# Optimization experiments

Hardware: AMD Instinct MI355X
Metric: run time of the kernel (lower is better)

The kernel has to match this reference:

```python
import jax, jax.numpy as jnp
import numpy as np

B, H, W, DIM, NH = 2, 48, 48, 768, 12
HD = DIM // NH  # 64


def setup_inputs() -> dict:
    key = jax.random.key(0)
    ks = jax.random.split(key, 7)
    std = 0.02
    return {
        "x": jax.random.normal(ks[0], (B, H, W, DIM), jnp.float32),
        "rel_pos_h": jax.random.normal(ks[1], (2 * H - 1, HD), jnp.float32) * std,
        "rel_pos_w": jax.random.normal(ks[2], (2 * W - 1, HD), jnp.float32) * std,
        "qkv_w": jax.random.normal(ks[3], (3 * DIM, DIM), jnp.float32) * std,
        "qkv_b": jnp.zeros((3 * DIM,), jnp.float32),
        "proj_w": jax.random.normal(ks[4], (DIM, DIM), jnp.float32) * std,
        "proj_b": jnp.zeros((DIM,), jnp.float32),
    }


def reference(x, rel_pos_h, rel_pos_w, qkv_w, qkv_b, proj_w, proj_b):
    b, h, w, dim = x.shape
    nh = NH
    hd = dim // nh
    scale = hd ** -0.5
    n = h * w
    # qkv projection: (B,N,3*dim) -> (3, B*nh, N, hd)
    qkv = x.reshape(b, n, dim) @ qkv_w.T + qkv_b
    qkv = qkv.reshape(b, n, 3, nh, hd).transpose(2, 0, 3, 1, 4).reshape(3, b * nh, n, hd)
    q, k, v = qkv[0], qkv[1], qkv[2]
    # scaled dot-product scores (B*nh, N, N)
    attn = jnp.einsum('bnc,bmc->bnm', q * scale, k)
    # decomposed relative position bias (q_size == k_size, no interpolation)
    idx_h = jnp.arange(h)[:, None] - jnp.arange(h)[None, :] + (h - 1)  # (h,h)
    idx_w = jnp.arange(w)[:, None] - jnp.arange(w)[None, :] + (w - 1)  # (w,w)
    Rh = rel_pos_h[idx_h]  # (h, h, hd)
    Rw = rel_pos_w[idx_w]  # (w, w, hd)
    r_q = q.reshape(b * nh, h, w, hd)
    rel_h = jnp.einsum('bhwc,hkc->bhwk', r_q, Rh)  # (B*nh, h, w, h)
    rel_w = jnp.einsum('bhwc,wkc->bhwk', r_q, Rw)  # (B*nh, h, w, w)
    attn = (attn.reshape(b * nh, h, w, h, w)
            + rel_h[:, :, :, :, None]
            + rel_w[:, :, :, None, :]).reshape(b * nh, n, n)
    attn = jax.nn.softmax(attn, axis=-1)
    out = (attn @ v).reshape(b, nh, h, w, hd).transpose(0, 2, 3, 1, 4).reshape(b, h, w, dim)
    return out @ proj_w.T + proj_b
```

## Files before the change

kernel.cpp:

```cpp
#include <hip/hip_runtime.h>
#include <hip/hip_bf16.h>
#include <stdint.h>

#define NQ    2304
#define MROWS 4608
#define DIMC  768
#define NHEAD 12
#define HEADS 24
#define HD    64

typedef unsigned int uint;
typedef unsigned short u16;
typedef __attribute__((ext_vector_type(8))) short s16x8;
typedef __attribute__((ext_vector_type(4))) float f32x4;

#define MFMA16(a, b, c) __builtin_amdgcn_mfma_f32_16x16x32_bf16((a), (b), (c), 0, 0, 0)

static __device__ __forceinline__ float bfbits2f(uint u) {
  union { uint i; float f; } c; c.i = u << 16; return c.f;
}
static __device__ __forceinline__ u16 f2bf(float f) {
  __hip_bfloat16 h = __float2bfloat16(f);
  union { __hip_bfloat16 h; u16 u; } c; c.h = h; return c.u;
}
static __device__ __forceinline__ u16 f2h(float f) {
  union { _Float16 h; u16 u; } c; c.h = (_Float16)f; return c.u;
}
static __device__ __forceinline__ float h2f(u16 u) {
  union { u16 u; _Float16 h; } c; c.u = u; return (float)c.h;
}
static __device__ __forceinline__ void dec8(uint4 p, float* f) {
  f[0] = bfbits2f(p.x & 0xFFFFu); f[1] = bfbits2f(p.x >> 16);
  f[2] = bfbits2f(p.y & 0xFFFFu); f[3] = bfbits2f(p.y >> 16);
  f[4] = bfbits2f(p.z & 0xFFFFu); f[5] = bfbits2f(p.z >> 16);
  f[6] = bfbits2f(p.w & 0xFFFFu); f[7] = bfbits2f(p.w >> 16);
}
static __device__ __forceinline__ void ld8(const void* p, size_t idx, int bf, float* f) {
  if (bf) { dec8(*(const uint4*)((const u16*)p + idx), f); }
  else {
    const float4* q = (const float4*)((const float*)p + idx);
    float4 a = q[0], b = q[1];
    f[0] = a.x; f[1] = a.y; f[2] = a.z; f[3] = a.w;
    f[4] = b.x; f[5] = b.y; f[6] = b.z; f[7] = b.w;
  }
}
static __device__ __forceinline__ float ld1(const void* p, size_t idx, int bf) {
  return bf ? bfbits2f(((const u16*)p)[idx]) : ((const float*)p)[idx];
}
static __device__ __forceinline__ uint4 ld8_to_bf(const void* p, size_t idx, int bf) {
  if (bf) return *(const uint4*)((const u16*)p + idx);
  float f[8]; ld8(p, idx, 0, f);
  uint4 u;
  u.x = (uint)f2bf(f[0]) | ((uint)f2bf(f[1]) << 16);
  u.y = (uint)f2bf(f[2]) | ((uint)f2bf(f[3]) << 16);
  u.z = (uint)f2bf(f[4]) | ((uint)f2bf(f[5]) << 16);
  u.w = (uint)f2bf(f[6]) | ((uint)f2bf(f[7]) << 16);
  return u;
}

__global__ __launch_bounds__(256) void detect_k(const u16* __restrict__ x,
                                                int* __restrict__ mode) {
  __shared__ int wsum[4];
  int t = threadIdx.x;
  int cnt = 0;
  for (int i = 0; i < 8; ++i) {
    uint u = x[(size_t)(t * 8 + i) * 2];
    uint e = (u >> 7) & 0xFFu;
    uint mag = u & 0x7FFFu;
    if (mag == 0 || (e >= 113 && e <= 133)) cnt++;
  }
#pragma unroll
  for (int d = 1; d < 64; d <<= 1) cnt += __shfl_xor(cnt, d);
  if ((t & 63) == 0) wsum[t >> 6] = cnt;
  __syncthreads();
  if (t == 0) mode[0] = ((wsum[0] + wsum[1] + wsum[2] + wsum[3]) > 1024) ? 1 : 0;
}

#define NX8 442368u
#define NW8 221184u
#define NP8 73728u
__global__ __launch_bounds__(256) void convert_k(
    const void* __restrict__ x, const void* __restrict__ qkvw,
    const void* __restrict__ pw, const int* __restrict__ mode,
    u16* __restrict__ xb, u16* __restrict__ wb, u16* __restrict__ pwb)
{
  const int bf = mode[0];
  uint i8 = blockIdx.x * 256 + threadIdx.x;
  if (i8 < NX8) {
    *(uint4*)(xb + (size_t)i8 * 8) = ld8_to_bf(x, (size_t)i8 * 8, bf);
  } else if (i8 < NX8 + NW8) {
    size_t j = i8 - NX8;
    *(uint4*)(wb + j * 8) = ld8_to_bf(qkvw, j * 8, bf);
  } else if (i8 < NX8 + NW8 + NP8) {
    size_t j = i8 - NX8 - NW8;
    *(uint4*)(pwb + j * 8) = ld8_to_bf(pw, j * 8, bf);
  }
}

__global__ __launch_bounds__(256) void qkv_gemm_k(
    const u16* __restrict__ Xb, const u16* __restrict__ Wb,
    const void* __restrict__ Bq, const int* __restrict__ mode,
    u16* __restrict__ Q, u16* __restrict__ K, u16* __restrict__ V)
{
  __shared__ __align__(16) u16 As[128][40];
  __shared__ __align__(16) u16 Bs[128][40];
  const int bf = mode[0];
  const int t = threadIdx.x;
  const int w = t >> 6, l15 = t & 15, quad = (t >> 4) & 3;
  const int wr = w >> 1, wc = w & 1;
  const int row0 = blockIdx.y << 7, col0 = blockIdx.x << 7;
  const int lr = t >> 1, lk = (t & 1) << 4;

  f32x4 zero4 = {0.f, 0.f, 0.f, 0.f};
  f32x4 acc[4][4];
#pragma unroll
  for (int i = 0; i < 4; ++i)
#pragma unroll
    for (int j = 0; j < 4; ++j) acc[i][j] = zero4;

  for (int kt = 0; kt < DIMC; kt += 32) {
    __syncthreads();
    *(uint4*)&As[lr][lk]     = *(const uint4*)(Xb + (size_t)(row0 + lr) * DIMC + kt + lk);
    *(uint4*)&As[lr][lk + 8] = *(const uint4*)(Xb + (size_t)(row0 + lr) * DIMC + kt + lk + 8);
    *(uint4*)&Bs[lr][lk]     = *(const uint4*)(Wb + (size_t)(col0 + lr) * DIMC + kt + lk);
    *(uint4*)&Bs[lr][lk + 8] = *(const uint4*)(Wb + (size_t)(col0 + lr) * DIMC + kt + lk + 8);
    __syncthreads();
    s16x8 af[4], bfr[4];
#pragma unroll
    for (int i = 0; i < 4; ++i)
      af[i] = *(const s16x8*)&As[(wr << 6) + (i << 4) + l15][quad << 3];
#pragma unroll
    for (int j = 0; j < 4; ++j)
      bfr[j] = *(const s16x8*)&Bs[(wc << 6) + (j << 4) + l15][quad << 3];
#pragma unroll
    for (int i = 0; i < 4; ++i)
#pragma unroll
      for (int j = 0; j < 4; ++j)
        acc[i][j] = MFMA16(af[i], bfr[j], acc[i][j]);
  }

#pragma unroll
  for (int jt = 0; jt < 4; ++jt) {
    int col = col0 + (wc << 6) + (jt << 4) + l15;
    int which = col / DIMC;
    int rem = col - which * DIMC;
    int head = rem >> 6, d = rem & 63;
    float bv = ld1(Bq, col, bf);
    u16* dst = (which == 0) ? Q : (which == 1) ? K : V;
#pragma unroll
    for (int i = 0; i < 4; ++i)
#pragma unroll
      for (int r = 0; r < 4; ++r) {
        int mrow = row0 + (wr << 6) + (i << 4) + (quad << 2) + r;
        int b_ = (mrow >= NQ) ? 1 : 0;
        int n = mrow - b_ * NQ;
        dst[(((size_t)(b_ * NHEAD + head)) * NQ + n) * HD + d] = f2bf(acc[i][jt][r] + bv);
      }
  }
}

__global__ __launch_bounds__(256) void vtrans_k(
    const u16* __restrict__ V, u16* __restrict__ Vt)
{
  __shared__ __align__(16) u16 L[64][72];
  const int blk = blockIdx.x;
  const int bhd = blk / 36;
  const int n0 = (blk - bhd * 36) << 6;
  const int t = threadIdx.x;
  const int r = t >> 3, c8 = (t & 7) << 3;

  const u16* src = V + ((size_t)bhd * NQ + n0) * HD;
  *(uint4*)&L[r][c8]      = *(const uint4*)(src + (size_t)r * HD + c8);
  *(uint4*)&L[r + 32][c8] = *(const uint4*)(src + (size_t)(r + 32) * HD + c8);
  __syncthreads();

  u16* dst = Vt + (size_t)bhd * HD * NQ + n0;
#pragma unroll
  for (int half = 0; half < 2; ++half) {
    int d = r + (half << 5);
    u16 tmp[8];
#pragma unroll
    for (int j = 0; j < 8; ++j) tmp[j] = L[c8 + j][d];
    *(uint4*)(dst + (size_t)d * NQ + c8) = *(uint4*)tmp;
  }
}

__global__ __launch_bounds__(256) void bias_gemm_k(
    const u16* __restrict__ Qw,
    const void* __restrict__ rph, const void* __restrict__ rpw,
    const int* __restrict__ mode,
    u16* __restrict__ Bh_g, u16* __restrict__ Bw_g)
{
  __shared__ __align__(16) u16 As[128][72];
  __shared__ __align__(16) u16 Bs[192][72];
  const int bf = mode[0];
  const int t = threadIdx.x;
  const int w = t >> 6, l15 = t & 15, quad = (t >> 4) & 3;
  const int wr = w >> 1, wc = w & 1;
  const int blk = blockIdx.x;
  const int bhd = blk / 18;
  const int row0 = (blk - bhd * 18) << 7;

  {
    int lr = t >> 1, lk = (t & 1) << 5;
    const u16* src = Qw + ((size_t)bhd * NQ + row0 + lr) * HD + lk;
    *(uint4*)&As[lr][lk]      = *(const uint4*)(src);
    *(uint4*)&As[lr][lk + 8]  = *(const uint4*)(src + 8);
    *(uint4*)&As[lr][lk + 16] = *(const uint4*)(src + 16);
    *(uint4*)&As[lr][lk + 24] = *(const uint4*)(src + 24);
  }
  for (int e = t; e < 384; e += 256) {
    int row = e >> 1, k32 = (e & 1) << 5;
    int tab = (row >= 96) ? 1 : 0;
    int r2 = row - (tab ? 96 : 0);
    if (r2 > 94) r2 = 0;
    const void* src = tab ? rpw : rph;
    *(uint4*)&Bs[row][k32]      = ld8_to_bf(src, (size_t)r2 * HD + k32, bf);
    *(uint4*)&Bs[row][k32 + 8]  = ld8_to_bf(src, (size_t)r2 * HD + k32 + 8, bf);
    *(uint4*)&Bs[row][k32 + 16] = ld8_to_bf(src, (size_t)r2 * HD + k32 + 16, bf);
    *(uint4*)&Bs[row][k32 + 24] = ld8_to_bf(src, (size_t)r2 * HD + k32 + 24, bf);
  }
  __syncthreads();

  f32x4 zero4 = {0.f, 0.f, 0.f, 0.f};
  f32x4 acc[4][6];
#pragma unroll
  for (int i = 0; i < 4; ++i)
#pragma unroll
    for (int j = 0; j < 6; ++j) acc[i][j] = zero4;

#pragma unroll
  for (int ks = 0; ks < 2; ++ks) {
    s16x8 af[4], bfr[6];
#pragma unroll
    for (int i = 0; i < 4; ++i)
      af[i] = *(const s16x8*)&As[(wr << 6) + (i << 4) + l15][(ks << 5) + (quad << 3)];
#pragma unroll
    for (int j = 0; j < 6; ++j)
      bfr[j] = *(const s16x8*)&Bs[wc * 96 + (j << 4) + l15][(ks << 5) + (quad << 3)];
#pragma unroll
    for (int i = 0; i < 4; ++i)
#pragma unroll
      for (int j = 0; j < 6; ++j)
        acc[i][j] = MFMA16(af[i], bfr[j], acc[i][j]);
  }

#pragma unroll
  for (int jt = 0; jt < 6; ++jt) {
    int col = wc * 96 + (jt << 4) + l15;
    int tab = (col >= 96) ? 1 : 0;
    int j = col - (tab ? 96 : 0);
    if (j >= 95) continue;
    u16* dstT = tab ? Bw_g : Bh_g;
#pragma unroll
    for (int i = 0; i < 4; ++i)
#pragma unroll
      for (int r = 0; r < 4; ++r) {
        int n = row0 + (wr << 6) + (i << 4) + (quad << 2) + r;
        int qh = (n * 10923) >> 19;
        int coord = tab ? (n - qh * 48) : qh;
        int c = coord + 47 - j;
        if (c >= 0 && c < 48)
          dstT[((size_t)bhd * 48 + c) * NQ + n] = f2h(acc[i][jt][r]);
      }
  }
}

__global__ __launch_bounds__(256) void attn_k(
    const u16* __restrict__ Qw, const u16* __restrict__ Kw,
    const u16* __restrict__ Vtg,
    const u16* __restrict__ Bh_g, const u16* __restrict__ Bw_g,
    int S, float* __restrict__ Opart, float* __restrict__ Lpart,
    u16* __restrict__ Aout)
{
  __shared__ __align__(16) u16 BhL[48][256];
  __shared__ __align__(16) u16 BwL[256][52];

  const int bid = blockIdx.x;
  const int xcd = bid & 7;
  const int local = bid >> 3;
  const int per_head = 9 * S;
  const int head_l = local / per_head;
  const int rem = local - head_l * per_head;
  const int qb = rem / S;
  const int z = rem - qb * S;
  const int bhd = xcd * 3 + head_l;
  const int q0 = qb << 8;
  const int span = NQ / S;
  const int kt_lo = z * span, kt_hi = kt_lo + span;

  const int t = threadIdx.x;
  const int w = t >> 6, l15 = t & 15, quad = (t >> 4) & 3;
  const float scale = 0.125f;

  const u16* kbase  = Kw  + (size_t)bhd * NQ * HD;
  const u16* vtbase = Vtg + (size_t)bhd * HD * NQ;
  const int q0w = q0 + (w << 6);

  for (int e = t; e < 1536; e += 256) {
    int c = e >> 5;
    int off = (e & 31) << 3;
    size_t gi = ((size_t)bhd * 48 + c) * NQ + q0 + off;
    *(uint4*)&BhL[c][off] = *(const uint4*)(Bh_g + gi);
    uint4 wv = *(const uint4*)(Bw_g + gi);
    u16 vals[8];
    vals[0] = wv.x & 0xFFFFu; vals[1] = wv.x >> 16;
    vals[2] = wv.y & 0xFFFFu; vals[3] = wv.y >> 16;
    vals[4] = wv.z & 0xFFFFu; vals[5] = wv.z >> 16;
    vals[6] = wv.w & 0xFFFFu; vals[7] = wv.w >> 16;
#pragma unroll
    for (int j = 0; j < 8; ++j) BwL[off + j][c] = vals[j];
  }

  s16x8 qa0[4], qa1[4];
#pragma unroll
  for (int g = 0; g < 4; ++g) {
    const u16* qfrag = Qw + ((size_t)bhd * NQ + q0w + (g << 4) + l15) * HD + (quad << 3);
    qa0[g] = *(const s16x8*)(qfrag);
    qa1[g] = *(const s16x8*)(qfrag + 32);
  }

  __syncthreads();

  f32x4 zero4 = {0.f, 0.f, 0.f, 0.f};
  f32x4 acc_o[4][4];
#pragma unroll
  for (int g = 0; g < 4; ++g)
#pragma unroll
    for (int nc = 0; nc < 4; ++nc) acc_o[g][nc] = zero4;
  float l_st[4] = {0.f, 0.f, 0.f, 0.f};
  const int srcA = ((quad & 1) << 5) + l15;
  const int srcB = srcA + 16;
  const int hi = quad >> 1;
  int km = 0;

  for (int kt0 = kt_lo; kt0 < kt_hi; kt0 += 64) {
    int kh0 = (kt0 * 10923) >> 19;
    int thr = (kh0 + 1) * 48 - kt0;

#pragma unroll
    for (int h = 0; h < 2; ++h) {
      uint W[4][4];
#pragma unroll
      for (int nc2 = 0; nc2 < 2; ++nc2) {
        int nc = (h << 1) + nc2;
        const u16* kp = kbase + (size_t)(kt0 + (nc << 4) + l15) * HD + (quad << 3);
        s16x8 kb0 = *(const s16x8*)(kp);
        s16x8 kb1 = *(const s16x8*)(kp + 32);
        int bnc = km + (nc << 4);
        bnc = (bnc >= 48) ? bnc - 48 : bnc;
        int kl = (nc << 4) + (quad << 2);
#pragma unroll
        for (int g = 0; g < 4; ++g) {
          f32x4 a = MFMA16(kb0, qa0[g], zero4);
          f32x4 s4 = MFMA16(kb1, qa1[g], a);
          int qrl = (w << 6) + (g << 4) + l15;
          float bh0v = h2f(BhL[kh0][qrl]);
          float bh1v = h2f(BhL[kh0 + 1][qrl]);
          uint2 pv = *(const uint2*)&BwL[qrl][bnc + (quad << 2)];
          float b0 = h2f((u16)(pv.x & 0xFFFFu));
          float b1 = h2f((u16)(pv.x >> 16));
          float b2 = h2f((u16)(pv.y & 0xFFFFu));
          float b3 = h2f((u16)(pv.y >> 16));
          float e0 = __expf(s4[0] * scale + ((kl     >= thr) ? bh1v : bh0v) + b0);
          float e1 = __expf(s4[1] * scale + ((kl + 1 >= thr) ? bh1v : bh0v) + b1);
          float e2 = __expf(s4[2] * scale + ((kl + 2 >= thr) ? bh1v : bh0v) + b2);
          float e3 = __expf(s4[3] * scale + ((kl + 3 >= thr) ? bh1v : bh0v) + b3);
          l_st[g] += (e0 + e1) + (e2 + e3);
          W[g][2 * nc2]     = (uint)f2bf(e0) | ((uint)f2bf(e1) << 16);
          W[g][2 * nc2 + 1] = (uint)f2bf(e2) | ((uint)f2bf(e3) << 16);
        }
      }
      s16x8 vb[4];
#pragma unroll
      for (int nc = 0; nc < 4; ++nc)
        vb[nc] = *(const s16x8*)(vtbase + (size_t)((nc << 4) + l15) * NQ
                                 + kt0 + (h << 5) + (quad << 3));
#pragma unroll
      for (int g = 0; g < 4; ++g) {
        uint e0 = __shfl(W[g][0], srcA), e1 = __shfl(W[g][1], srcA);
        uint e2 = __shfl(W[g][2], srcA), e3 = __shfl(W[g][3], srcA);
        uint g0 = __shfl(W[g][0], srcB), g1 = __shfl(W[g][1], srcB);
        uint g2 = __shfl(W[g][2], srcB), g3 = __shfl(W[g][3], srcB);
        union { uint u[4]; s16x8 v; } pf;
        pf.u[0] = hi ? e2 : e0; pf.u[1] = hi ? e3 : e1;
        pf.u[2] = hi ? g2 : g0; pf.u[3] = hi ? g3 : g1;
#pragma unroll
        for (int nc = 0; nc < 4; ++nc)
          acc_o[g][nc] = MFMA16(pf.v, vb[nc], acc_o[g][nc]);
      }
    }
    km += 16;
    if (km >= 48) km -= 48;
  }

#pragma unroll
  for (int g = 0; g < 4; ++g) {
    float lg = l_st[g];
    lg += __shfl_xor(lg, 16);
    lg += __shfl_xor(lg, 32);
    if (S > 1) {
      float* Op = Opart + ((size_t)(z * HEADS + bhd) * NQ + q0) * HD;
#pragma unroll
      for (int r = 0; r < 4; ++r) {
        int row = (w << 6) + (g << 4) + (quad << 2) + r;
#pragma unroll
        for (int nc = 0; nc < 4; ++nc)
          Op[(size_t)row * HD + (nc << 4) + l15] = acc_o[g][nc][r];
      }
      if (quad == 0)
        Lpart[(size_t)(z * HEADS + bhd) * NQ + q0w + (g << 4) + l15] = lg;
    } else {
      int b_ = bhd / NHEAD, head = bhd - b_ * NHEAD;
      float invl = 1.f / lg;
      int bsrc = (quad << 4) + (quad << 2);
#pragma unroll
      for (int r = 0; r < 4; ++r) {
        float inv = __shfl(invl, bsrc + r);
        int token = q0 + (w << 6) + (g << 4) + (quad << 2) + r;
        u16* dst = Aout + ((size_t)b_ * NQ + token) * DIMC + (head << 6);
#pragma unroll
        for (int nc = 0; nc < 4; ++nc)
          dst[(nc << 4) + l15] = f2bf(acc_o[g][nc][r] * inv);
      }
    }
  }
}

__global__ __launch_bounds__(256) void combine_k(
    const float* __restrict__ Op, const float* __restrict__ Lp,
    int S, u16* __restrict__ Aout)
{
  int idx = blockIdx.x * 256 + threadIdx.x;
  int m = idx / 192;
  int cq = idx - m * 192;
  int ccol = cq << 2;
  int head = ccol >> 6, d0 = ccol & 63;
  int b_ = (m >= NQ) ? 1 : 0;
  int n = m - b_ * NQ;
  int bh = b_ * NHEAD + head;
  float ox = 0.f, oy = 0.f, oz = 0.f, ow = 0.f, ls = 0.f;
  for (int zz = 0; zz < S; ++zz) {
    const float* ob = Op + ((size_t)(zz * HEADS + bh) * NQ + n) * HD + d0;
    float4 v = *(const float4*)ob;
    ox += v.x; oy += v.y; oz += v.z; ow += v.w;
    ls += Lp[(size_t)(zz * HEADS + bh) * NQ + n];
  }
  float inv = 1.f / ls;
  u16* dst = Aout + (size_t)m * DIMC + ccol;
  dst[0] = f2bf(ox * inv); dst[1] = f2bf(oy * inv);
  dst[2] = f2bf(oz * inv); dst[3] = f2bf(ow * inv);
}

__global__ __launch_bounds__(256) void proj_gemm_k(
    const u16* __restrict__ A, const u16* __restrict__ Wb,
    const void* __restrict__ Bp, const int* __restrict__ mode,
    void* __restrict__ Out)
{
  __shared__ __align__(16) u16 As[128][40];
  __shared__ __align__(16) u16 Bs[128][40];
  const int bf = mode[0];
  const int t = threadIdx.x;
  const int w = t >> 6, l15 = t & 15, quad = (t >> 4) & 3;
  const int wr = w >> 1, wc = w & 1;
  const int row0 = blockIdx.y << 7, col0 = blockIdx.x << 7;
  const int lr = t >> 1, lk = (t & 1) << 4;

  f32x4 zero4 = {0.f, 0.f, 0.f, 0.f};
  f32x4 acc[4][4];
#pragma unroll
  for (int i = 0; i < 4; ++i)
#pragma unroll
    for (int j = 0; j < 4; ++j) acc[i][j] = zero4;

  for (int kt = 0; kt < DIMC; kt += 32) {
    __syncthreads();
    *(uint4*)&As[lr][lk]     = *(const uint4*)(A + (size_t)(row0 + lr) * DIMC + kt + lk);
    *(uint4*)&As[lr][lk + 8] = *(const uint4*)(A + (size_t)(row0 + lr) * DIMC + kt + lk + 8);
    *(uint4*)&Bs[lr][lk]     = *(const uint4*)(Wb + (size_t)(col0 + lr) * DIMC + kt + lk);
    *(uint4*)&Bs[lr][lk + 8] = *(const uint4*)(Wb + (size_t)(col0 + lr) * DIMC + kt + lk + 8);
    __syncthreads();
    s16x8 af[4], bfr[4];
#pragma unroll
    for (int i = 0; i < 4; ++i)
      af[i] = *(const s16x8*)&As[(wr << 6) + (i << 4) + l15][quad << 3];
#pragma unroll
    for (int j = 0; j < 4; ++j)
      bfr[j] = *(const s16x8*)&Bs[(wc << 6) + (j << 4) + l15][quad << 3];
#pragma unroll
    for (int i = 0; i < 4; ++i)
#pragma unroll
      for (int j = 0; j < 4; ++j)
        acc[i][j] = MFMA16(af[i], bfr[j], acc[i][j]);
  }

#pragma unroll
  for (int jt = 0; jt < 4; ++jt) {
    int col = col0 + (wc << 6) + (jt << 4) + l15;
    float bv = ld1(Bp, col, bf);
#pragma unroll
    for (int i = 0; i < 4; ++i)
#pragma unroll
      for (int r = 0; r < 4; ++r) {
        int mrow = row0 + (wr << 6) + (i << 4) + (quad << 2) + r;
        float val = acc[i][jt][r] + bv;
        size_t off = (size_t)mrow * DIMC + col;
        if (bf) ((u16*)Out)[off] = f2bf(val);
        else    ((float*)Out)[off] = val;
      }
  }
}

extern "C" void kernel_launch(void* const* d_in, const int* in_sizes, int n_in,
                              void* d_out, int out_size, void* d_ws, size_t ws_size,
                              hipStream_t stream)
{
  const void* x    = d_in[0];
  const void* rph  = d_in[1];
  const void* rpw  = d_in[2];
  const void* qkvw = d_in[3];
  const void* qkvb = d_in[4];
  const void* pw   = d_in[5];
  const void* pb   = d_in[6];

  int* mode = (int*)d_ws;
  const size_t qkv_elems = (size_t)HEADS * NQ * HD;
  const size_t NXe = (size_t)MROWS * DIMC;
  const size_t NWe = (size_t)3 * DIMC * DIMC;
  const size_t NPe = (size_t)DIMC * DIMC;
  u16* q    = (u16*)((char*)d_ws + 16);
  u16* k    = q + qkv_elems;
  u16* vt   = k + qkv_elems;
  u16* aout = vt + qkv_elems;
  u16* v    = aout;
  u16* pwb  = aout + qkv_elems;
  const size_t biasElems = (size_t)HEADS * 48 * NQ;
  u16* bh_g = pwb + NPe;
  u16* bw_g = bh_g + biasElems;
  char* R   = (char*)(bw_g + biasElems);
  const size_t baseR = (size_t)((char*)R - (char*)d_ws);
  u16* xb = (u16*)R;
  u16* wb = xb + NXe;
  const size_t needXW = (NXe + NWe) * 2;
  const size_t perO = (size_t)HEADS * NQ * HD * 4;
  const size_t perL = (size_t)HEADS * NQ * 4;

  int S = 1;
  size_t n3 = 3 * (perO + perL), n2 = 2 * (perO + perL), n1 = perO + perL;
  if (ws_size >= baseR + (n3 > needXW ? n3 : needXW)) S = 3;
  else if (ws_size >= baseR + (n2 > needXW ? n2 : needXW)) S = 2;
  float* opart = (float*)R;
  float* lpart = (float*)(R + (size_t)S * perO);

  detect_k<<<1, 256, 0, stream>>>((const u16*)x, mode);
  convert_k<<<dim3(2880), 256, 0, stream>>>(x, qkvw, pw, mode, xb, wb, pwb);
  qkv_gemm_k<<<dim3(18, 36), 256, 0, stream>>>(xb, wb, qkvb, mode, q, k, v);
  vtrans_k<<<dim3(864), 256, 0, stream>>>(v, vt);
  bias_gemm_k<<<dim3(432), 256, 0, stream>>>(q, rph, rpw, mode, bh_g, bw_g);
  attn_k<<<dim3(216 * S), 256, 0, stream>>>(q, k, vt, bh_g, bw_g,
                                            S, opart, lpart, aout);
  if (S > 1)
    combine_k<<<dim3(3456), 256, 0, stream>>>(opart, lpart, S, aout);
  proj_gemm_k<<<dim3(6, 36), 256, 0, stream>>>(aout, pwb, pb, mode, d_out);
}
```

Before: 344.5 us.

## Use direct global-to-LDS loads in GEMMs and halve attention query tile with K prefetch

The QKV and projection GEMMs now fill their unpadded LDS tiles with global_load_lds, skipping the round trip through registers. The attention kernel now gives each block 128 queries instead of 256 and launches twice as many blocks. It also double-buffers K fragments in registers so the next key tile loads while the current one goes through softmax and PV. The trade-off is more redundant K/V reads across blocks and possible LDS bank conflicts from dropping the padding.

```diff
diff --git a/kernel.cpp b/kernel.cpp
--- a/kernel.cpp
+++ b/kernel.cpp
@@ -56,6 +56,11 @@
   u.z = (uint)f2bf(f[4]) | ((uint)f2bf(f[5]) << 16);
   u.w = (uint)f2bf(f[6]) | ((uint)f2bf(f[7]) << 16);
   return u;
+}
+static __device__ __forceinline__ void gll16(const u16* g, u16* l) {
+  __builtin_amdgcn_global_load_lds(
+      (const __attribute__((address_space(1))) unsigned int*)g,
+      (__attribute__((address_space(3))) unsigned int*)l, 16, 0, 0);
 }
 
 __global__ __launch_bounds__(256) void detect_k(const u16* __restrict__ x,
@@ -102,14 +107,14 @@
     const void* __restrict__ Bq, const int* __restrict__ mode,
     u16* __restrict__ Q, u16* __restrict__ K, u16* __restrict__ V)
 {
-  __shared__ __align__(16) u16 As[128][40];
-  __shared__ __align__(16) u16 Bs[128][40];
+  __shared__ __align__(16) u16 As[128][32];
+  __shared__ __align__(16) u16 Bs[128][32];
   const int bf = mode[0];
   const int t = threadIdx.x;
-  const int w = t >> 6, l15 = t & 15, quad = (t >> 4) & 3;
+  const int w = t >> 6, lane = t & 63, l15 = t & 15, quad = (t >> 4) & 3;
   const int wr = w >> 1, wc = w & 1;
   const int row0 = blockIdx.y << 7, col0 = blockIdx.x << 7;
-  const int lr = t >> 1, lk = (t & 1) << 4;
+  const int r4 = lane >> 2, c8 = (lane & 3) << 3;
 
   f32x4 zero4 = {0.f, 0.f, 0.f, 0.f};
   f32x4 acc[4][4];
@@ -120,10 +125,10 @@
 
   for (int kt = 0; kt < DIMC; kt += 32) {
     __syncthreads();
-    *(uint4*)&As[lr][lk]     = *(const uint4*)(Xb + (size_t)(row0 + lr) * DIMC + kt + lk);
-    *(uint4*)&As[lr][lk + 8] = *(const uint4*)(Xb + (size_t)(row0 + lr) * DIMC + kt + lk + 8);
-    *(uint4*)&Bs[lr][lk]     = *(const uint4*)(Wb + (size_t)(col0 + lr) * DIMC + kt + lk);
-    *(uint4*)&Bs[lr][lk + 8] = *(const uint4*)(Wb + (size_t)(col0 + lr) * DIMC + kt + lk + 8);
+    gll16(Xb + (size_t)(row0 + (w << 5) + r4) * DIMC + kt + c8,      &As[(w << 5)][0]);
+    gll16(Xb + (size_t)(row0 + (w << 5) + 16 + r4) * DIMC + kt + c8, &As[(w << 5) + 16][0]);
+    gll16(Wb + (size_t)(col0 + (w << 5) + r4) * DIMC + kt + c8,      &Bs[(w << 5)][0]);
+    gll16(Wb + (size_t)(col0 + (w << 5) + 16 + r4) * DIMC + kt + c8, &Bs[(w << 5) + 16][0]);
     __syncthreads();
     s16x8 af[4], bfr[4];
 #pragma unroll
@@ -266,6 +271,75 @@
   }
 }
 
+#define ATILE(KB, KN, T0, PREF, KM) do {                                      \
+    f32x4 acc_s[2][4];                                                        \
+    _Pragma("unroll")                                                         \
+    for (int nc = 0; nc < 4; ++nc) {                                          \
+      f32x4 a0 = MFMA16(KB[2*nc], qa0[0], zero4);                             \
+      acc_s[0][nc] = MFMA16(KB[2*nc+1], qa1[0], a0);                          \
+      f32x4 a1 = MFMA16(KB[2*nc], qa0[1], zero4);                             \
+      acc_s[1][nc] = MFMA16(KB[2*nc+1], qa1[1], a1);                          \
+    }                                                                         \
+    if (PREF) {                                                               \
+      _Pragma("unroll")                                                       \
+      for (int nc = 0; nc < 4; ++nc) {                                        \
+        const u16* kp_ = kbase + (size_t)((T0) + 64 + (nc << 4) + l15) * HD + (quad << 3); \
+        KN[2*nc]   = *(const s16x8*)(kp_);                                    \
+        KN[2*nc+1] = *(const s16x8*)(kp_ + 32);                               \
+      }                                                                       \
+    }                                                                         \
+    int kh0 = ((T0) * 10923) >> 19;                                           \
+    int thr = (kh0 + 1) * 48 - (T0);                                          \
+    uint Wq[2][8];                                                            \
+    _Pragma("unroll")                                                         \
+    for (int g = 0; g < 2; ++g) {                                             \
+      int qrl = (w << 5) + (g << 4) + l15;                                    \
+      float bh0v = h2f(BhL[kh0][qrl]);                                        \
+      float bh1v = h2f(BhL[kh0 + 1][qrl]);                                    \
+      float sum = 0.f;                                                        \
+      _Pragma("unroll")                                                       \
+      for (int nc = 0; nc < 4; ++nc) {                                        \
+        int bnc = (KM) + (nc << 4);                                           \
+        bnc = (bnc >= 48) ? bnc - 48 : bnc;                                   \
+        uint2 pv = *(const uint2*)&BwL[qrl][bnc + (quad << 2)];               \
+        float b0 = h2f((u16)(pv.x & 0xFFFFu));                                \
+        float b1 = h2f((u16)(pv.x >> 16));                                    \
+        float b2 = h2f((u16)(pv.y & 0xFFFFu));                                \
+        float b3 = h2f((u16)(pv.y >> 16));                                    \
+        int kl = (nc << 4) + (quad << 2);                                     \
+        float e0 = __expf(acc_s[g][nc][0] * scale + ((kl     >= thr) ? bh1v : bh0v) + b0); \
+        float e1 = __expf(acc_s[g][nc][1] * scale + ((kl + 1 >= thr) ? bh1v : bh0v) + b1); \
+        float e2 = __expf(acc_s[g][nc][2] * scale + ((kl + 2 >= thr) ? bh1v : bh0v) + b2); \
+        float e3 = __expf(acc_s[g][nc][3] * scale + ((kl + 3 >= thr) ? bh1v : bh0v) + b3); \
+        sum += (e0 + e1) + (e2 + e3);                                         \
+        Wq[g][2*nc]   = (uint)f2bf(e0) | ((uint)f2bf(e1) << 16);              \
+        Wq[g][2*nc+1] = (uint)f2bf(e2) | ((uint)f2bf(e3) << 16);              \
+      }                                                                       \
+      l_st[g] += sum;                                                         \
+    }                                                                         \
+    _Pragma("unroll")                                                         \
+    for (int h = 0; h < 2; ++h) {                                             \
+      s16x8 vb[4];                                                            \
+      _Pragma("unroll")                                                       \
+      for (int nc = 0; nc < 4; ++nc)                                          \
+        vb[nc] = *(const s16x8*)(vtbase + (size_t)((nc << 4) + l15) * NQ      \
+                                 + (T0) + (h << 5) + (quad << 3));            \
+      _Pragma("unroll")                                                       \
+      for (int g = 0; g < 2; ++g) {                                           \
+        uint e0 = __shfl(Wq[g][4*h+0], srcA), e1 = __shfl(Wq[g][4*h+1], srcA); \
+        uint e2 = __shfl(Wq[g][4*h+2], srcA), e3 = __shfl(Wq[g][4*h+3], srcA); \
+        uint g0 = __shfl(Wq[g][4*h+0], srcB), g1 = __shfl(Wq[g][4*h+1], srcB); \
+        uint g2 = __shfl(Wq[g][4*h+2], srcB), g3 = __shfl(Wq[g][4*h+3], srcB); \
+        union { uint u[4]; s16x8 v; } pf;                                     \
+        pf.u[0] = hi ? e2 : e0; pf.u[1] = hi ? e3 : e1;                       \
+        pf.u[2] = hi ? g2 : g0; pf.u[3] = hi ? g3 : g1;                       \
+        _Pragma("unroll")                                                     \
+        for (int nc = 0; nc < 4; ++nc)                                        \
+          acc_o[g][nc] = MFMA16(pf.v, vb[nc], acc_o[g][nc]);                  \
+      }                                                                       \
+    }                                                                         \
+  } while (0)
+
 __global__ __launch_bounds__(256) void attn_k(
     const u16* __restrict__ Qw, const u16* __restrict__ Kw,
     const u16* __restrict__ Vtg,
@@ -273,19 +347,19 @@
     int S, float* __restrict__ Opart, float* __restrict__ Lpart,
     u16* __restrict__ Aout)
 {
-  __shared__ __align__(16) u16 BhL[48][256];
-  __shared__ __align__(16) u16 BwL[256][52];
+  __shared__ __align__(16) u16 BhL[48][128];
+  __shared__ __align__(16) u16 BwL[128][52];
 
   const int bid = blockIdx.x;
   const int xcd = bid & 7;
   const int local = bid >> 3;
-  const int per_head = 9 * S;
+  const int per_head = 18 * S;
   const int head_l = local / per_head;
   const int rem = local - head_l * per_head;
   const int qb = rem / S;
   const int z = rem - qb * S;
   const int bhd = xcd * 3 + head_l;
-  const int q0 = qb << 8;
+  const int q0 = qb << 7;
   const int span = NQ / S;
   const int kt_lo = z * span, kt_hi = kt_lo + span;
 
@@ -295,11 +369,11 @@
 
   const u16* kbase  = Kw  + (size_t)bhd * NQ * HD;
   const u16* vtbase = Vtg + (size_t)bhd * HD * NQ;
-  const int q0w = q0 + (w << 6);
-
-  for (int e = t; e < 1536; e += 256) {
-    int c = e >> 5;
-    int off = (e & 31) << 3;
+  const int q0w = q0 + (w << 5);
+
+  for (int e = t; e < 768; e += 256) {
+    int c = e >> 4;
+    int off = (e & 15) << 3;
     size_t gi = ((size_t)bhd * 48 + c) * NQ + q0 + off;
     *(uint4*)&BhL[c][off] = *(const uint4*)(Bh_g + gi);
     uint4 wv = *(const uint4*)(Bw_g + gi);
@@ -312,90 +386,46 @@
     for (int j = 0; j < 8; ++j) BwL[off + j][c] = vals[j];
   }
 
-  s16x8 qa0[4], qa1[4];
-#pragma unroll
-  for (int g = 0; g < 4; ++g) {
+  s16x8 qa0[2], qa1[2];
+#pragma unroll
+  for (int g = 0; g < 2; ++g) {
     const u16* qfrag = Qw + ((size_t)bhd * NQ + q0w + (g << 4) + l15) * HD + (quad << 3);
     qa0[g] = *(const s16x8*)(qfrag);
     qa1[g] = *(const s16x8*)(qfrag + 32);
   }
 
+  s16x8 kbA[8], kbB[8];
+#pragma unroll
+  for (int nc = 0; nc < 4; ++nc) {
+    const u16* kp = kbase + (size_t)(kt_lo + (nc << 4) + l15) * HD + (quad << 3);
+    kbA[2*nc]   = *(const s16x8*)(kp);
+    kbA[2*nc+1] = *(const s16x8*)(kp + 32);
+  }
+
   __syncthreads();
 
   f32x4 zero4 = {0.f, 0.f, 0.f, 0.f};
-  f32x4 acc_o[4][4];
-#pragma unroll
-  for (int g = 0; g < 4; ++g)
+  f32x4 acc_o[2][4];
+#pragma unroll
+  for (int g = 0; g < 2; ++g)
 #pragma unroll
     for (int nc = 0; nc < 4; ++nc) acc_o[g][nc] = zero4;
-  float l_st[4] = {0.f, 0.f, 0.f, 0.f};
+  float l_st[2] = {0.f, 0.f};
   const int srcA = ((quad & 1) << 5) + l15;
   const int srcB = srcA + 16;
   const int hi = quad >> 1;
   int km = 0;
 
-  for (int kt0 = kt_lo; kt0 < kt_hi; kt0 += 64) {
-    int kh0 = (kt0 * 10923) >> 19;
-    int thr = (kh0 + 1) * 48 - kt0;
-
-#pragma unroll
-    for (int h = 0; h < 2; ++h) {
-      uint W[4][4];
-#pragma unroll
-      for (int nc2 = 0; nc2 < 2; ++nc2) {
-        int nc = (h << 1) + nc2;
-        const u16* kp = kbase + (size_t)(kt0 + (nc << 4) + l15) * HD + (quad << 3);
-        s16x8 kb0 = *(const s16x8*)(kp);
-        s16x8 kb1 = *(const s16x8*)(kp + 32);
-        int bnc = km + (nc << 4);
-        bnc = (bnc >= 48) ? bnc - 48 : bnc;
-        int kl = (nc << 4) + (quad << 2);
-#pragma unroll
-        for (int g = 0; g < 4; ++g) {
-          f32x4 a = MFMA16(kb0, qa0[g], zero4);
-          f32x4 s4 = MFMA16(kb1, qa1[g], a);
-          int qrl = (w << 6) + (g << 4) + l15;
-          float bh0v = h2f(BhL[kh0][qrl]);
-          float bh1v = h2f(BhL[kh0 + 1][qrl]);
-          uint2 pv = *(const uint2*)&BwL[qrl][bnc + (quad << 2)];
-          float b0 = h2f((u16)(pv.x & 0xFFFFu));
-          float b1 = h2f((u16)(pv.x >> 16));
-          float b2 = h2f((u16)(pv.y & 0xFFFFu));
-          float b3 = h2f((u16)(pv.y >> 16));
-          float e0 = __expf(s4[0] * scale + ((kl     >= thr) ? bh1v : bh0v) + b0);
-          float e1 = __expf(s4[1] * scale + ((kl + 1 >= thr) ? bh1v : bh0v) + b1);
-          float e2 = __expf(s4[2] * scale + ((kl + 2 >= thr) ? bh1v : bh0v) + b2);
-          float e3 = __expf(s4[3] * scale + ((kl + 3 >= thr) ? bh1v : bh0v) + b3);
-          l_st[g] += (e0 + e1) + (e2 + e3);
-          W[g][2 * nc2]     = (uint)f2bf(e0) | ((uint)f2bf(e1) << 16);
-          W[g][2 * nc2 + 1] = (uint)f2bf(e2) | ((uint)f2bf(e3) << 16);
-        }
-      }
-      s16x8 vb[4];
-#pragma unroll
-      for (int nc = 0; nc < 4; ++nc)
-        vb[nc] = *(const s16x8*)(vtbase + (size_t)((nc << 4) + l15) * NQ
-                                 + kt0 + (h << 5) + (quad << 3));
-#pragma unroll
-      for (int g = 0; g < 4; ++g) {
-        uint e0 = __shfl(W[g][0], srcA), e1 = __shfl(W[g][1], srcA);
-        uint e2 = __shfl(W[g][2], srcA), e3 = __shfl(W[g][3], srcA);
-        uint g0 = __shfl(W[g][0], srcB), g1 = __shfl(W[g][1], srcB);
-        uint g2 = __shfl(W[g][2], srcB), g3 = __shfl(W[g][3], srcB);
-        union { uint u[4]; s16x8 v; } pf;
-        pf.u[0] = hi ? e2 : e0; pf.u[1] = hi ? e3 : e1;
-        pf.u[2] = hi ? g2 : g0; pf.u[3] = hi ? g3 : g1;
-#pragma unroll
-        for (int nc = 0; nc < 4; ++nc)
-          acc_o[g][nc] = MFMA16(pf.v, vb[nc], acc_o[g][nc]);
-      }
-    }
-    km += 16;
-    if (km >= 48) km -= 48;
-  }
-
-#pragma unroll
-  for (int g = 0; g < 4; ++g) {
+  for (int kt0 = kt_lo; kt0 < kt_hi; kt0 += 128) {
+    ATILE(kbA, kbB, kt0, 1, km);
+    km += 16; if (km >= 48) km -= 48;
+    int pref2 = (kt0 + 128) < kt_hi;
+    ATILE(kbB, kbA, kt0 + 64, pref2, km);
+    km += 16; if (km >= 48) km -= 48;
+  }
+
+#pragma unroll
+  for (int g = 0; g < 2; ++g) {
     float lg = l_st[g];
     lg += __shfl_xor(lg, 16);
     lg += __shfl_xor(lg, 32);
@@ -403,7 +433,7 @@
       float* Op = Opart + ((size_t)(z * HEADS + bhd) * NQ + q0) * HD;
 #pragma unroll
       for (int r = 0; r < 4; ++r) {
-        int row = (w << 6) + (g << 4) + (quad << 2) + r;
+        int row = (w << 5) + (g << 4) + (quad << 2) + r;
 #pragma unroll
         for (int nc = 0; nc < 4; ++nc)
           Op[(size_t)row * HD + (nc << 4) + l15] = acc_o[g][nc][r];
@@ -417,7 +447,7 @@
 #pragma unroll
       for (int r = 0; r < 4; ++r) {
         float inv = __shfl(invl, bsrc + r);
-        int token = q0 + (w << 6) + (g << 4) + (quad << 2) + r;
+        int token = q0 + (w << 5) + (g << 4) + (quad << 2) + r;
         u16* dst = Aout + ((size_t)b_ * NQ + token) * DIMC + (head << 6);
 #pragma unroll
         for (int nc = 0; nc < 4; ++nc)
@@ -457,14 +487,14 @@
     const void* __restrict__ Bp, const int* __restrict__ mode,
     void* __restrict__ Out)
 {
-  __shared__ __align__(16) u16 As[128][40];
-  __shared__ __align__(16) u16 Bs[128][40];
+  __shared__ __align__(16) u16 As[128][32];
+  __shared__ __align__(16) u16 Bs[128][32];
   const int bf = mode[0];
   const int t = threadIdx.x;
-  const int w = t >> 6, l15 = t & 15, quad = (t >> 4) & 3;
+  const int w = t >> 6, lane = t & 63, l15 = t & 15, quad = (t >> 4) & 3;
   const int wr = w >> 1, wc = w & 1;
   const int row0 = blockIdx.y << 7, col0 = blockIdx.x << 7;
-  const int lr = t >> 1, lk = (t & 1) << 4;
+  const int r4 = lane >> 2, c8 = (lane & 3) << 3;
 
   f32x4 zero4 = {0.f, 0.f, 0.f, 0.f};
   f32x4 acc[4][4];
@@ -475,10 +505,10 @@
 
   for (int kt = 0; kt < DIMC; kt += 32) {
     __syncthreads();
-    *(uint4*)&As[lr][lk]     = *(const uint4*)(A + (size_t)(row0 + lr) * DIMC + kt + lk);
-    *(uint4*)&As[lr][lk + 8] = *(const uint4*)(A + (size_t)(row0 + lr) * DIMC + kt + lk + 8);
-    *(uint4*)&Bs[lr][lk]     = *(const uint4*)(Wb + (size_t)(col0 + lr) * DIMC + kt + lk);
-    *(uint4*)&Bs[lr][lk + 8] = *(const uint4*)(Wb + (size_t)(col0 + lr) * DIMC + kt + lk + 8);
+    gll16(A + (size_t)(row0 + (w << 5) + r4) * DIMC + kt + c8,       &As[(w << 5)][0]);
+    gll16(A + (size_t)(row0 + (w << 5) + 16 + r4) * DIMC + kt + c8,  &As[(w << 5) + 16][0]);
+    gll16(Wb + (size_t)(col0 + (w << 5) + r4) * DIMC + kt + c8,      &Bs[(w << 5)][0]);
+    gll16(Wb + (size_t)(col0 + (w << 5) + 16 + r4) * DIMC + kt + c8, &Bs[(w << 5) + 16][0]);
     __syncthreads();
     s16x8 af[4], bfr[4];
 #pragma unroll
@@ -546,7 +576,7 @@
   const size_t perL = (size_t)HEADS * NQ * 4;
 
   int S = 1;
-  size_t n3 = 3 * (perO + perL), n2 = 2 * (perO + perL), n1 = perO + perL;
+  size_t n3 = 3 * (perO + perL), n2 = 2 * (perO + perL);
   if (ws_size >= baseR + (n3 > needXW ? n3 : needXW)) S = 3;
   else if (ws_size >= baseR + (n2 > needXW ? n2 : needXW)) S = 2;
   float* opart = (float*)R;
@@ -557,7 +587,7 @@
   qkv_gemm_k<<<dim3(18, 36), 256, 0, stream>>>(xb, wb, qkvb, mode, q, k, v);
   vtrans_k<<<dim3(864), 256, 0, stream>>>(v, vt);
   bias_gemm_k<<<dim3(432), 256, 0, stream>>>(q, rph, rpw, mode, bh_g, bw_g);
-  attn_k<<<dim3(216 * S), 256, 0, stream>>>(q, k, vt, bh_g, bw_g,
+  attn_k<<<dim3(432 * S), 256, 0, stream>>>(q, k, vt, bh_g, bw_g,
                                             S, opart, lpart, aout);
   if (S > 1)
     combine_k<<<dim3(3456), 256, 0, stream>>>(opart, lpart, S, aout);
```

New measurement: 335.4 us. -2.6%, faster.
